# Optimization experiments

Measured on AMD Instinct MI355X. Metric: run time of the kernel, lower is better.

Reference implementation:

```python
import jax, jax.numpy as jnp
import numpy as np

H, C, L = 2, 32, 25
EPS = 1e-5


def setup_inputs() -> dict:
    key = jax.random.key(0)
    ks = jax.random.split(key, 12)
    N, E = 20000, 100000
    x_input = jax.random.normal(ks[0], (N, 5), jnp.float32)
    # edges with no self loops (module uses add_self_loops=True, which first removes them)
    src = jax.random.randint(ks[1], (L, E), 0, N, dtype=jnp.int32)
    off = jax.random.randint(ks[2], (L, E), 1, N, dtype=jnp.int32)
    dst = (src + off) % N
    edge_indices = jnp.stack([src, dst], axis=1)              # [L, 2, E]
    edge_weights = jax.random.uniform(ks[3], (L, E, 1), jnp.float32)
    g = lambda k, shp, fan: jax.random.normal(k, shp, jnp.float32) / np.float32(np.sqrt(fan))
    return {
        "x_input": x_input,
        "edge_indices": edge_indices,
        "edge_weights": edge_weights,
        "Wl": g(ks[4], (L, 5, H * C), 5),
        "bl": jnp.zeros((L, H * C), jnp.float32),
        "Wr": g(ks[5], (L, 5, H * C), 5),
        "br": jnp.zeros((L, H * C), jnp.float32),
        "We": g(ks[6], (L, 1, H * C), 1),
        "att": g(ks[7], (L, H, C), C),
        "conv_bias": jnp.zeros((L, C), jnp.float32),
        "gamma1": jnp.ones((L, C), jnp.float32),
        "beta1": jnp.zeros((L, C), jnp.float32),
        "W1": g(ks[8], (800, 800), 800),
        "b1": jnp.zeros((800,), jnp.float32),
        "W2": g(ks[9], (800, 5), 800),
        "b2": jnp.zeros((5,), jnp.float32),
    }


def reference(x_input, edge_indices, edge_weights, Wl, bl, Wr, br, We, att,
              conv_bias, gamma1, beta1, W1, b1, W2, b2):
    N = x_input.shape[0]
    loops = jnp.arange(N, dtype=edge_indices.dtype)

    def layer(carry, p):
        ei, ew, wl, bl_, wr, br_, we, a, cb, g_, be_ = p
        src, dst = ei[0], ei[1]
        ones_e = jnp.ones((src.shape[0],), x_input.dtype)
        # add_self_loops with fill_value='mean': loop attr = mean of incoming edge attrs
        cnt = jax.ops.segment_sum(ones_e, dst, num_segments=N)
        loop_attr = jax.ops.segment_sum(ew, dst, num_segments=N) / jnp.maximum(cnt, 1.0)[:, None]
        s2 = jnp.concatenate([src, loops])
        d2 = jnp.concatenate([dst, loops])
        ea = jnp.concatenate([ew, loop_attr], axis=0)          # [E+N, 1]
        xl = (x_input @ wl + bl_).reshape(N, H, C)             # source transform
        xr = (x_input @ wr + br_).reshape(N, H, C)             # target transform
        eh = jax.nn.leaky_relu(xl[s2] + xr[d2] + (ea @ we).reshape(-1, H, C), 0.2)
        alpha = jnp.einsum('ehc,hc->eh', eh, a)                # [E+N, H]
        amax = jax.ops.segment_max(alpha, d2, num_segments=N)
        alpha = jnp.exp(alpha - amax[d2])
        alpha = alpha / jax.ops.segment_sum(alpha, d2, num_segments=N)[d2]
        msg = (xl[s2] * alpha[:, :, None]).reshape(-1, H * C)
        deg = jax.ops.segment_sum(jnp.ones((s2.shape[0],), x_input.dtype), d2, num_segments=N)
        out = (jax.ops.segment_sum(msg, d2, num_segments=N) / deg[:, None]).reshape(N, H, C)
        out = out.mean(axis=1) + cb                            # concat=False -> mean over heads, + bias
        mu = out.mean(axis=0)
        var = out.var(axis=0)                                  # BatchNorm1d, training-mode batch stats
        out = g_ * (out - mu) * jax.lax.rsqrt(var + EPS) + be_
        return carry, jax.nn.leaky_relu(out, 0.01)

    _, hs = jax.lax.scan(layer, None,
                         (edge_indices, edge_weights, Wl, bl, Wr, br, We, att,
                          conv_bias, gamma1, beta1))            # [L, N, C]
    h = jnp.transpose(hs, (1, 0, 2)).reshape(N, L * C)          # cat along feature dim
    h = jax.nn.relu(h @ W1 + b1)
    return h @ W2 + b2
```

## Files before the change

kernel.cpp:

```cpp
#include <hip/hip_runtime.h>
#include <hip/hip_bf16.h>

#define N_NODES 20000
#define N_EDGES 100000
#define N_LAYERS 25
#define NPAD 20096
#define EPS_BN 1e-5f
#define LOG2E 1.44269504088896340736f
#define NL_NN (N_LAYERS * N_NODES)
#define TOTAL_E (N_LAYERS * N_EDGES)
#define SCAN_BLKS ((NL_NN + 1023) / 1024)
#define QUARTER_N 5000
#define CNT_BLKS (N_LAYERS * 4)
#define XLR_BASE CNT_BLKS
#define XLR_BLKS (NL_NN / 16)
#define W1T_BASE (XLR_BASE + XLR_BLKS)
#define PREP_BLKS (W1T_BASE + 700)
#define EDGE_BLKS ((TOTAL_E + 1023) / 1024)
#define FILL_BLKS (EDGE_BLKS + SCAN_BLKS)
#define NGRP 14
#define ATTN_BLKS (NL_NN / 4)
#define ATTN_PER_XCD (ATTN_BLKS / 8)

typedef short short8 __attribute__((ext_vector_type(8)));
typedef short short4v __attribute__((ext_vector_type(4)));
typedef float floatx4 __attribute__((ext_vector_type(4)));
typedef int int8v __attribute__((ext_vector_type(8)));

template <int PAT>
__device__ __forceinline__ float swz(float v) {
  return __int_as_float(__builtin_amdgcn_ds_swizzle(__float_as_int(v), PAT));
}

template <int CTRL>
__device__ __forceinline__ float dpp_add(float v) {
  int r = __builtin_amdgcn_update_dpp(0, __float_as_int(v), CTRL, 0xF, 0xF, true);
  return v + __int_as_float(r);
}

__device__ __forceinline__ float ldbf(const unsigned short* __restrict__ p, int idx) {
  return __uint_as_float((unsigned)p[idx] << 16);
}

__device__ __forceinline__ unsigned short bfbits(float v) {
  return __builtin_bit_cast(unsigned short, (__hip_bfloat16)v);
}

__device__ __forceinline__ void gl_lds16(const short* g, short* l) {
  __builtin_amdgcn_global_load_lds(
      (const __attribute__((address_space(1))) void*)g,
      (__attribute__((address_space(3))) void*)l, 16, 0, 0);
}

__device__ __forceinline__ void sload8(const int2* p, int8v& ra, int8v& rb) {
  asm volatile(
      "s_load_dwordx8 %0, %2, 0x0\n\t"
      "s_load_dwordx8 %1, %2, 0x20\n\t"
      "s_waitcnt lgkmcnt(0)"
      : "=s"(ra), "=s"(rb)
      : "s"(p));
}

__device__ __forceinline__ void red8(float& p0, float& p1, float& p2, float& p3,
                                     float& p4, float& p5, float& p6, float& p7) {
  asm volatile(
      "s_nop 1\n\t"
      "v_add_f32_dpp %0, %0, %0 quad_perm:[1,0,3,2] row_mask:0xf bank_mask:0xf\n\t"
      "v_add_f32_dpp %1, %1, %1 quad_perm:[1,0,3,2] row_mask:0xf bank_mask:0xf\n\t"
      "v_add_f32_dpp %2, %2, %2 quad_perm:[1,0,3,2] row_mask:0xf bank_mask:0xf\n\t"
      "v_add_f32_dpp %3, %3, %3 quad_perm:[1,0,3,2] row_mask:0xf bank_mask:0xf\n\t"
      "v_add_f32_dpp %4, %4, %4 quad_perm:[1,0,3,2] row_mask:0xf bank_mask:0xf\n\t"
      "v_add_f32_dpp %5, %5, %5 quad_perm:[1,0,3,2] row_mask:0xf bank_mask:0xf\n\t"
      "v_add_f32_dpp %6, %6, %6 quad_perm:[1,0,3,2] row_mask:0xf bank_mask:0xf\n\t"
      "v_add_f32_dpp %7, %7, %7 quad_perm:[1,0,3,2] row_mask:0xf bank_mask:0xf\n\t"
      "v_add_f32_dpp %0, %0, %0 quad_perm:[2,3,0,1] row_mask:0xf bank_mask:0xf\n\t"
      "v_add_f32_dpp %1, %1, %1 quad_perm:[2,3,0,1] row_mask:0xf bank_mask:0xf\n\t"
      "v_add_f32_dpp %2, %2, %2 quad_perm:[2,3,0,1] row_mask:0xf bank_mask:0xf\n\t"
      "v_add_f32_dpp %3, %3, %3 quad_perm:[2,3,0,1] row_mask:0xf bank_mask:0xf\n\t"
      "v_add_f32_dpp %4, %4, %4 quad_perm:[2,3,0,1] row_mask:0xf bank_mask:0xf\n\t"
      "v_add_f32_dpp %5, %5, %5 quad_perm:[2,3,0,1] row_mask:0xf bank_mask:0xf\n\t"
      "v_add_f32_dpp %6, %6, %6 quad_perm:[2,3,0,1] row_mask:0xf bank_mask:0xf\n\t"
      "v_add_f32_dpp %7, %7, %7 quad_perm:[2,3,0,1] row_mask:0xf bank_mask:0xf\n\t"
      "v_add_f32_dpp %0, %0, %0 row_half_mirror row_mask:0xf bank_mask:0xf\n\t"
      "v_add_f32_dpp %1, %1, %1 row_half_mirror row_mask:0xf bank_mask:0xf\n\t"
      "v_add_f32_dpp %2, %2, %2 row_half_mirror row_mask:0xf bank_mask:0xf\n\t"
      "v_add_f32_dpp %3, %3, %3 row_half_mirror row_mask:0xf bank_mask:0xf\n\t"
      "v_add_f32_dpp %4, %4, %4 row_half_mirror row_mask:0xf bank_mask:0xf\n\t"
      "v_add_f32_dpp %5, %5, %5 row_half_mirror row_mask:0xf bank_mask:0xf\n\t"
      "v_add_f32_dpp %6, %6, %6 row_half_mirror row_mask:0xf bank_mask:0xf\n\t"
      "v_add_f32_dpp %7, %7, %7 row_half_mirror row_mask:0xf bank_mask:0xf\n\t"
      "v_add_f32_dpp %0, %0, %0 row_mirror row_mask:0xf bank_mask:0xf\n\t"
      "v_add_f32_dpp %1, %1, %1 row_mirror row_mask:0xf bank_mask:0xf\n\t"
      "v_add_f32_dpp %2, %2, %2 row_mirror row_mask:0xf bank_mask:0xf\n\t"
      "v_add_f32_dpp %3, %3, %3 row_mirror row_mask:0xf bank_mask:0xf\n\t"
      "v_add_f32_dpp %4, %4, %4 row_mirror row_mask:0xf bank_mask:0xf\n\t"
      "v_add_f32_dpp %5, %5, %5 row_mirror row_mask:0xf bank_mask:0xf\n\t"
      "v_add_f32_dpp %6, %6, %6 row_mirror row_mask:0xf bank_mask:0xf\n\t"
      "v_add_f32_dpp %7, %7, %7 row_mirror row_mask:0xf bank_mask:0xf\n\t"
      "s_nop 1"
      : "+v"(p0), "+v"(p1), "+v"(p2), "+v"(p3),
        "+v"(p4), "+v"(p5), "+v"(p6), "+v"(p7));
}

__device__ __forceinline__ float red1(float p) {
  asm volatile(
      "s_nop 1\n\t"
      "v_add_f32_dpp %0, %0, %0 quad_perm:[1,0,3,2] row_mask:0xf bank_mask:0xf\n\t"
      "s_nop 1\n\t"
      "v_add_f32_dpp %0, %0, %0 quad_perm:[2,3,0,1] row_mask:0xf bank_mask:0xf\n\t"
      "s_nop 1\n\t"
      "v_add_f32_dpp %0, %0, %0 row_half_mirror row_mask:0xf bank_mask:0xf\n\t"
      "s_nop 1\n\t"
      "v_add_f32_dpp %0, %0, %0 row_mirror row_mask:0xf bank_mask:0xf\n\t"
      "s_nop 1"
      : "+v"(p));
  return p;
}

__global__ __launch_bounds__(1024) void prep_kernel(
    const int* __restrict__ ei, const float* __restrict__ x,
    const float* __restrict__ Wl, const float* __restrict__ bl,
    const float* __restrict__ Wr, const float* __restrict__ br,
    const float* __restrict__ W1, int* __restrict__ cnt,
    int* __restrict__ rank,
    unsigned short* __restrict__ xlb, unsigned short* __restrict__ xrb,
    __hip_bfloat16* __restrict__ W1bT) {
  __shared__ int smem[QUARTER_N];
  int b = blockIdx.x;
  if (b < XLR_BASE) {
    int l = b >> 2, base = (b & 3) * QUARTER_N;
    for (int i = threadIdx.x; i < QUARTER_N; i += 1024) smem[i] = 0;
    __syncthreads();
    const int* dstp = ei + (size_t)l * 2 * N_EDGES + N_EDGES;
    int* rkp = rank + l * N_EDGES;
    for (int e = threadIdx.x; e < N_EDGES; e += 1024) {
      int d = dstp[e] - base;
      if ((unsigned)d < (unsigned)QUARTER_N) rkp[e] = atomicAdd(&smem[d], 1);
    }
    __syncthreads();
    int* outp = cnt + l * N_NODES + base;
    for (int i = threadIdx.x; i < QUARTER_N; i += 1024) outp[i] = smem[i];
  } else if (b < W1T_BASE) {
    int wid = (b - XLR_BASE) * 16 + (threadIdx.x >> 6);
    int lane = threadIdx.x & 63;
    int l = wid / N_NODES, n = wid - l * N_NODES;
    float a = bl[l * 64 + lane];
    float c = br[l * 64 + lane];
#pragma unroll
    for (int k = 0; k < 5; k++) {
      float xk = x[n * 5 + k];
      a = fmaf(xk, Wl[(l * 5 + k) * 64 + lane], a);
      c = fmaf(xk, Wr[(l * 5 + k) * 64 + lane], c);
    }
    xlb[wid * 64 + lane] = bfbits(a);
    xrb[wid * 64 + lane] = bfbits(c);
  } else {
    float* tile = (float*)smem;
    int bb = b - W1T_BASE;
    int j0 = (bb % 28) * 32, k0 = (bb / 28) * 32;
    int tx = threadIdx.x & 31, ty = threadIdx.x >> 5;
    tile[ty * 33 + tx] = (j0 + tx < 800) ? W1[(k0 + ty) * 800 + j0 + tx] : 0.f;
    __syncthreads();
    W1bT[(size_t)(j0 + ty) * 800 + k0 + tx] = (__hip_bfloat16)tile[tx * 33 + ty];
  }
}

__global__ __launch_bounds__(1024) void scan_a(const int* __restrict__ cnt,
                                               int* __restrict__ scn,
                                               int* __restrict__ btot,
                                               float* __restrict__ gsum,
                                               float* __restrict__ gsumsq) {
  int t = threadIdx.x, b = blockIdx.x;
  int i = b * 1024 + t;
  int lane = t & 63, wv = t >> 6;
  int v = (i < NL_NN) ? cnt[i] : 0;
  int sc = v;
#pragma unroll
  for (int off = 1; off < 64; off <<= 1) {
    int u = __shfl_up(sc, off);
    if (lane >= off) sc += u;
  }
  __shared__ int ws[16];
  if (lane == 63) ws[wv] = sc;
  __syncthreads();
  if (t < 16) {
    int xx = ws[t];
#pragma unroll
    for (int off = 1; off < 16; off <<= 1) {
      int u = __shfl_up(xx, off);
      if (t >= off) xx += u;
    }
    ws[t] = xx;
  }
  __syncthreads();
  int bofs = wv ? ws[wv - 1] : 0;
  if (i < NL_NN) scn[i] = bofs + sc - v;
  if (t == 0) btot[b] = ws[15];
  if (b == 200 && t < N_LAYERS * 32) {
    gsum[t] = 0.f;
    gsumsq[t] = 0.f;
  }
}

__global__ __launch_bounds__(512) void scan_b(const int* __restrict__ btot,
                                              int* __restrict__ boff) {
  int t = threadIdx.x;
  int lane = t & 63, wv = t >> 6;
  int v = (t < SCAN_BLKS) ? btot[t] : 0;
  int sc = v;
#pragma unroll
  for (int off = 1; off < 64; off <<= 1) {
    int u = __shfl_up(sc, off);
    if (lane >= off) sc += u;
  }
  __shared__ int ws[8];
  if (lane == 63) ws[wv] = sc;
  __syncthreads();
  if (t < 8) {
    int xx = ws[t];
#pragma unroll
    for (int off = 1; off < 8; off <<= 1) {
      int u = __shfl_up(xx, off);
      if (t >= off) xx += u;
    }
    ws[t] = xx;
  }
  __syncthreads();
  int bofs = wv ? ws[wv - 1] : 0;
  if (t < SCAN_BLKS) boff[t] = bofs + sc - v;
}

__global__ __launch_bounds__(1024) void fill_kernel(const int* __restrict__ ei,
                                                    const float* __restrict__ ew,
                                                    const int* __restrict__ scn,
                                                    const int* __restrict__ boff,
                                                    const int* __restrict__ rank,
                                                    int* __restrict__ rowfin,
                                                    int2* __restrict__ ep) {
  int b = blockIdx.x;
  if (b < EDGE_BLKS) {
    int idx = b * 1024 + threadIdx.x;
    if (idx >= TOTAL_E) return;
    int l = idx / N_EDGES, e = idx - l * N_EDGES;
    int src = ei[(size_t)l * 2 * N_EDGES + e];
    int dst = ei[(size_t)l * 2 * N_EDGES + N_EDGES + e];
    int g = l * N_NODES + dst;
    int pos = scn[g] + boff[g >> 10] + rank[idx];
    int2 rec;
    rec.x = src;
    rec.y = __float_as_int(ew[(size_t)l * N_EDGES + e]);
    ep[pos] = rec;
  } else {
    int i = (b - EDGE_BLKS) * 1024 + threadIdx.x;
    if (i < NL_NN) rowfin[i] = scn[i] + boff[i >> 10];
    if (i == 0) rowfin[NL_NN] = TOTAL_E;
    if (i < 8) {
      int2 z;
      z.x = 0;
      z.y = 0;
      ep[TOTAL_E + i] = z;
    }
  }
}

__global__ __launch_bounds__(256) void attn_kernel(
    const unsigned short* __restrict__ xlg, const unsigned short* __restrict__ xrg,
    const int* __restrict__ rowfin, const int2* __restrict__ ep,
    const float* __restrict__ We, const float* __restrict__ att,
    const float* __restrict__ cbias, unsigned short* __restrict__ out_pre) {
  int b = blockIdx.x;
  int nb = (b & 7) * ATTN_PER_XCD + (b >> 3);
  int wid = nb * 4 + (threadIdx.x >> 6);
  int lane = threadIdx.x & 63;
  int l = wid / N_NODES, n = wid - l * N_NODES;

  const unsigned short* xlb = xlg + (size_t)l * N_NODES * 64;
  float wev = We[l * 64 + lane];
  float att2v = att[l * 64 + lane] * LOG2E;

  float xrn = ldbf(xrg, wid * 64 + lane);
  float xln = ldbf(xlb, n * 64 + lane);

  int start = __builtin_amdgcn_readfirstlane(rowfin[wid]);
  int end   = __builtin_amdgcn_readfirstlane(rowfin[wid + 1]);
  int cnt = end - start;

  float ssum = 0.f, acc = 0.f, ewsum = 0.f;
  int nchunk = (cnt + 7) >> 3;
  for (int c = 0; c < nchunk; c++) {
    const int2* pchunk = ep + start + c * 8;
    int8v ra, rb;
    sload8(pchunk, ra, rb);
    int m = cnt - c * 8;
#define RECS(k) ((k) < 4 ? ra[2 * (k)] : rb[2 * ((k)-4)])
#define RECW(k) ((k) < 4 ? ra[2 * (k) + 1] : rb[2 * ((k)-4) + 1])
    float xa[8], pk[8], wv[8];
#pragma unroll
    for (int k = 0; k < 8; k++) {
      const unsigned short* ps = xlb + RECS(k) * 64;
      xa[k] = ldbf(ps, lane);
    }
#pragma unroll
    for (int k = 0; k < 8; k++) {
      bool ok = k < m;
      int wbits = ok ? RECW(k) : 0;
      wv[k] = __int_as_float(wbits);
      int bbits = ok ? 0 : (int)0xff800000;
      float bias = __int_as_float(bbits);
      float v = xa[k] + fmaf(wv[k], wev, xrn);
      float lk = fmaxf(v, 0.2f * v);
      pk[k] = fmaf(lk, att2v, bias);
    }
#undef RECS
#undef RECW
    red8(pk[0], pk[1], pk[2], pk[3], pk[4], pk[5], pk[6], pk[7]);
#pragma unroll
    for (int k = 0; k < 8; k++) pk[k] += swz<0x401F>(pk[k]);
#pragma unroll
    for (int k = 0; k < 8; k++) {
      float pe = __builtin_amdgcn_exp2f(pk[k]);
      ssum += pe;
      acc = fmaf(xa[k], pe, acc);
      ewsum += wv[k];
    }
  }
  {
    float w = ewsum * __builtin_amdgcn_rcpf(fmaxf((float)cnt, 1.f));
    float v = xln + fmaf(w, wev, xrn);
    float lk = fmaxf(v, 0.2f * v);
    float p = red1(lk * att2v);
    p += swz<0x401F>(p);
    float pe = __builtin_amdgcn_exp2f(p);
    ssum += pe;
    acc = fmaf(xln, pe, acc);
  }
  float outv = acc * __builtin_amdgcn_rcpf(ssum * (float)(cnt + 1));
  float o2 = outv + __shfl_xor(outv, 32);
  if (lane < 32)
    out_pre[wid * 32 + lane] = bfbits(0.5f * o2 + cbias[l * 32 + lane]);
}

__global__ __launch_bounds__(256) void stats_kernel(const unsigned short* __restrict__ out_pre,
                                                    float* __restrict__ gsum,
                                                    float* __restrict__ gsumsq) {
  int l = blockIdx.x >> 4, chunk = blockIdx.x & 15;
  int t = threadIdx.x;
  int c = t & 31, nsub = t >> 5;
  int n0 = chunk * 1250;
  float s1 = 0.f, s2 = 0.f;
  for (int n = n0 + nsub; n < n0 + 1250; n += 8) {
    float v = ldbf(out_pre, (l * N_NODES + n) * 32 + c);
    s1 += v; s2 += v * v;
  }
  __shared__ float l1[256], l2[256];
  l1[t] = s1; l2[t] = s2;
  __syncthreads();
  for (int off = 128; off >= 32; off >>= 1) {
    if (t < off) { l1[t] += l1[t + off]; l2[t] += l2[t + off]; }
    __syncthreads();
  }
  if (t < 32) {
    atomicAdd(&gsum[l * 32 + t], l1[t]);
    atomicAdd(&gsumsq[l * 32 + t], l2[t]);
  }
}

__global__ __launch_bounds__(256) void norm_kernel(const unsigned short* __restrict__ out_pre,
                                                   const float* __restrict__ gsum,
                                                   const float* __restrict__ gsumsq,
                                                   const float* __restrict__ gamma,
                                                   const float* __restrict__ beta,
                                                   unsigned short* __restrict__ hn) {
  int idx = blockIdx.x * 256 + threadIdx.x;
  int l = idx / (N_NODES * 8);
  int rem = idx - l * (N_NODES * 8);
  int n = rem >> 3, q = rem & 7;
  int c0 = q * 4;
  short4v v4 = *(const short4v*)(out_pre + (l * N_NODES + n) * 32 + c0);
  short4v o;
#pragma unroll
  for (int i = 0; i < 4; i++) {
    int c = c0 + i;
    float mu = gsum[l * 32 + c] * (1.f / N_NODES);
    float var = gsumsq[l * 32 + c] * (1.f / N_NODES) - mu * mu;
    float vv = __uint_as_float((unsigned)(unsigned short)v4[i] << 16);
    float v = gamma[l * 32 + c] * (vv - mu) * rsqrtf(var + EPS_BN) + beta[l * 32 + c];
    v = v > 0.f ? v : 0.01f * v;
    o[i] = (short)bfbits(v);
  }
  *(short4v*)(hn + ((size_t)l * NPAD + n) * 32 + c0) = o;
}

__global__ __launch_bounds__(256) void gemm1_kernel(const short* __restrict__ hn,
                                                    const short* __restrict__ W1bT,
                                                    const float* __restrict__ b1,
                                                    const float* __restrict__ W2,
                                                    float* __restrict__ p) {
  __shared__ __align__(16) short As[128 * 32];
  __shared__ __align__(16) short Bs[128 * 32];
  int t = threadIdx.x;
  int n0 = blockIdx.x * 128, m0 = blockIdx.y * 128;
  int wave = t >> 6, lane = t & 63;
  int wr = wave >> 1, wc = wave & 1;
  int mrow = lane & 15, quad = lane >> 4;
  floatx4 acc[4][4];
#pragma unroll
  for (int i = 0; i < 4; i++)
#pragma unroll
    for (int j = 0; j < 4; j++) acc[i][j] = (floatx4){0.f, 0.f, 0.f, 0.f};

  int r0 = t >> 2, s0 = t & 3;
  int r1 = (t + 256) >> 2, s1 = (t + 256) & 3;
  const short* aG0 = hn + (m0 + r0) * 32 + s0 * 8;
  const short* aG1 = hn + (m0 + r1) * 32 + s1 * 8;
  const short* bG0 = W1bT + (n0 + r0) * 800 + s0 * 8;
  const short* bG1 = W1bT + (n0 + r1) * 800 + s1 * 8;
  const int ak = NPAD * 32;
  short* aD0 = As + wave * 512;
  short* aD1 = As + 2048 + wave * 512;
  short* bD0 = Bs + wave * 512;
  short* bD1 = Bs + 2048 + wave * 512;

  for (int kt = 0; kt < 25; kt++) {
    gl_lds16(aG0, aD0);
    gl_lds16(aG1, aD1);
    gl_lds16(bG0, bD0);
    gl_lds16(bG1, bD1);
    aG0 += ak; aG1 += ak; bG0 += 32; bG1 += 32;
    __syncthreads();
    short8 af[4], bfr[4];
#pragma unroll
    for (int i = 0; i < 4; i++)
      af[i] = *(const short8*)(&As[(wr * 64 + i * 16 + mrow) * 32 + quad * 8]);
#pragma unroll
    for (int j = 0; j < 4; j++)
      bfr[j] = *(const short8*)(&Bs[(wc * 64 + j * 16 + mrow) * 32 + quad * 8]);
#pragma unroll
    for (int i = 0; i < 4; i++)
#pragma unroll
      for (int j = 0; j < 4; j++)
        acc[i][j] = __builtin_amdgcn_mfma_f32_16x16x32_bf16(af[i], bfr[j], acc[i][j], 0, 0, 0);
    __syncthreads();
  }

  float w2v[4][5];
  float b1v[4];
#pragma unroll
  for (int j = 0; j < 4; j++) {
    int col = n0 + wc * 64 + j * 16 + mrow;
    bool ok = col < 800;
    b1v[j] = ok ? b1[col] : 0.f;
#pragma unroll
    for (int jj = 0; jj < 5; jj++) w2v[j][jj] = ok ? W2[col * 5 + jj] : 0.f;
  }
  int grp = blockIdx.x * 2 + wc;
#pragma unroll
  for (int i = 0; i < 4; i++) {
#pragma unroll
    for (int r = 0; r < 4; r++) {
      float s[5] = {0.f, 0.f, 0.f, 0.f, 0.f};
#pragma unroll
      for (int j = 0; j < 4; j++) {
        float v = fmaxf(acc[i][j][r] + b1v[j], 0.f);
#pragma unroll
        for (int jj = 0; jj < 5; jj++) s[jj] = fmaf(v, w2v[j][jj], s[jj]);
      }
#pragma unroll
      for (int jj = 0; jj < 5; jj++) {
        s[jj] = dpp_add<0xB1>(s[jj]);
        s[jj] = dpp_add<0x4E>(s[jj]);
        s[jj] = dpp_add<0x141>(s[jj]);
        s[jj] = dpp_add<0x140>(s[jj]);
      }
      int row = m0 + wr * 64 + i * 16 + quad * 4 + r;
      if (mrow == 0) {
#pragma unroll
        for (int jj = 0; jj < 5; jj++)
          p[(row * NGRP + grp) * 5 + jj] = s[jj];
      }
    }
  }
}

__global__ __launch_bounds__(256) void gemm2r_kernel(const float* __restrict__ p,
                                                     const float* __restrict__ b2,
                                                     float* __restrict__ out) {
  int idx = blockIdx.x * 256 + threadIdx.x;
  if (idx >= N_NODES * 5) return;
  int row = idx / 5, jj = idx - row * 5;
  float s = b2[jj];
#pragma unroll
  for (int g = 0; g < NGRP; g++) s += p[(row * NGRP + g) * 5 + jj];
  out[idx] = s;
}

extern "C" void kernel_launch(void* const* d_in, const int* in_sizes, int n_in,
                              void* d_out, int out_size, void* d_ws, size_t ws_size,
                              hipStream_t stream) {
  const float* x    = (const float*)d_in[0];
  const int*   ei   = (const int*)d_in[1];
  const float* ew   = (const float*)d_in[2];
  const float* Wl   = (const float*)d_in[3];
  const float* bl   = (const float*)d_in[4];
  const float* Wr   = (const float*)d_in[5];
  const float* br   = (const float*)d_in[6];
  const float* We   = (const float*)d_in[7];
  const float* att  = (const float*)d_in[8];
  const float* cb   = (const float*)d_in[9];
  const float* gam  = (const float*)d_in[10];
  const float* bet  = (const float*)d_in[11];
  const float* W1   = (const float*)d_in[12];
  const float* b1   = (const float*)d_in[13];
  const float* W2   = (const float*)d_in[14];
  const float* b2   = (const float*)d_in[15];

  char* ws = (char*)d_ws;
  size_t off = 0;
  auto alloc = [&](size_t bytes) {
    void* p = ws + off;
    off = (off + bytes + 255) & ~(size_t)255;
    return p;
  };
  int* cnt     = (int*)alloc((size_t)NL_NN * 4);
  int* scn     = (int*)alloc((size_t)NL_NN * 4);
  int* btot    = (int*)alloc(SCAN_BLKS * 4);
  int* boff    = (int*)alloc(SCAN_BLKS * 4);
  int* rank    = (int*)alloc((size_t)TOTAL_E * 4);
  int* rowfin  = (int*)alloc((size_t)(NL_NN + 1) * 4);
  int2* ep     = (int2*)alloc((size_t)TOTAL_E * 8 + 64);
  unsigned short* out_pre = (unsigned short*)alloc((size_t)NL_NN * 32 * 2);
  float* gsum   = (float*)alloc(N_LAYERS * 32 * 4);
  float* gsumsq = (float*)alloc(N_LAYERS * 32 * 4);
  unsigned short* xlb = (unsigned short*)alloc((size_t)NL_NN * 64 * 2);
  unsigned short* xrb = (unsigned short*)alloc((size_t)NL_NN * 64 * 2);
  __hip_bfloat16* w1t = (__hip_bfloat16*)alloc((size_t)896 * 800 * 2);
  float* pbuf = (float*)alloc((size_t)NPAD * NGRP * 5 * 4);
  unsigned short* hn  = (unsigned short*)xlb;

  prep_kernel<<<PREP_BLKS, 1024, 0, stream>>>(ei, x, Wl, bl, Wr, br, W1,
                                              cnt, rank, xlb, xrb, w1t);
  scan_a<<<SCAN_BLKS, 1024, 0, stream>>>(cnt, scn, btot, gsum, gsumsq);
  scan_b<<<1, 512, 0, stream>>>(btot, boff);
  fill_kernel<<<FILL_BLKS, 1024, 0, stream>>>(ei, ew, scn, boff, rank, rowfin, ep);
  attn_kernel<<<ATTN_BLKS, 256, 0, stream>>>(
      xlb, xrb, rowfin, ep, We, att, cb, out_pre);
  stats_kernel<<<N_LAYERS * 16, 256, 0, stream>>>(out_pre, gsum, gsumsq);
  norm_kernel<<<(NL_NN * 8) / 256, 256, 0, stream>>>(
      out_pre, gsum, gsumsq, gam, bet, hn);
  gemm1_kernel<<<dim3(7, 157), 256, 0, stream>>>(
      (const short*)hn, (const short*)w1t, b1, W2, pbuf);
  gemm2r_kernel<<<(N_NODES * 5 + 255) / 256, 256, 0, stream>>>(
      pbuf, b2, (float*)d_out);
}
```

Baseline: 537.7 us.

## Recompute per-edge source projection from raw 5-dim inputs packed into edge records

Stops materializing the bf16 xl/xr projections (25 layers x 20000 nodes x 64). Each edge record in CSR order now carries the edge weight and the source node's 5 raw input features, and the attention kernel recomputes the 64-wide projection with 5 FMAs per lane. This removes a random 128-byte gather per edge and the large projection write, but edge records grow from 8 to 32 bytes and chunking drops from 8 to 4 edges. hn gets its own buffer, and its padding rows are now zeroed in prep because it no longer aliases xlb.

```diff
diff --git a/kernel.cpp b/kernel.cpp
--- a/kernel.cpp
+++ b/kernel.cpp
@@ -12,10 +12,10 @@
 #define SCAN_BLKS ((NL_NN + 1023) / 1024)
 #define QUARTER_N 5000
 #define CNT_BLKS (N_LAYERS * 4)
-#define XLR_BASE CNT_BLKS
-#define XLR_BLKS (NL_NN / 16)
-#define W1T_BASE (XLR_BASE + XLR_BLKS)
-#define PREP_BLKS (W1T_BASE + 700)
+#define W1T_END (CNT_BLKS + 700)
+#define XPAD_END (W1T_END + 157)
+#define HPAD_BLKS 75
+#define PREP_BLKS (XPAD_END + HPAD_BLKS)
 #define EDGE_BLKS ((TOTAL_E + 1023) / 1024)
 #define FILL_BLKS (EDGE_BLKS + SCAN_BLKS)
 #define NGRP 14
@@ -25,7 +25,9 @@
 typedef short short8 __attribute__((ext_vector_type(8)));
 typedef short short4v __attribute__((ext_vector_type(4)));
 typedef float floatx4 __attribute__((ext_vector_type(4)));
+typedef float float8v __attribute__((ext_vector_type(8)));
 typedef int int8v __attribute__((ext_vector_type(8)));
+typedef int int2v __attribute__((ext_vector_type(2)));
 
 template <int PAT>
 __device__ __forceinline__ float swz(float v) {
@@ -52,54 +54,60 @@
       (__attribute__((address_space(3))) void*)l, 16, 0, 0);
 }
 
-__device__ __forceinline__ void sload8(const int2* p, int8v& ra, int8v& rb) {
+__device__ __forceinline__ int8v sload8(const void* p) {
+  int8v r;
   asm volatile(
-      "s_load_dwordx8 %0, %2, 0x0\n\t"
-      "s_load_dwordx8 %1, %2, 0x20\n\t"
+      "s_load_dwordx8 %0, %1, 0x0\n\t"
       "s_waitcnt lgkmcnt(0)"
-      : "=s"(ra), "=s"(rb)
+      : "=s"(r)
       : "s"(p));
-}
-
-__device__ __forceinline__ void red8(float& p0, float& p1, float& p2, float& p3,
-                                     float& p4, float& p5, float& p6, float& p7) {
+  return r;
+}
+
+__device__ __forceinline__ void sload2(const void* p, int& a, int& b) {
+  int2v r;
+  asm volatile(
+      "s_load_dwordx2 %0, %1, 0x0\n\t"
+      "s_waitcnt lgkmcnt(0)"
+      : "=s"(r)
+      : "s"(p));
+  a = r[0];
+  b = r[1];
+}
+
+__device__ __forceinline__ void sload_chunk(const void* p, int8v& r0, int8v& r1,
+                                            int8v& r2, int8v& r3) {
+  asm volatile(
+      "s_load_dwordx8 %0, %4, 0x0\n\t"
+      "s_load_dwordx8 %1, %4, 0x20\n\t"
+      "s_load_dwordx8 %2, %4, 0x40\n\t"
+      "s_load_dwordx8 %3, %4, 0x60\n\t"
+      "s_waitcnt lgkmcnt(0)"
+      : "=s"(r0), "=s"(r1), "=s"(r2), "=s"(r3)
+      : "s"(p));
+}
+
+__device__ __forceinline__ void red4(float& p0, float& p1, float& p2, float& p3) {
   asm volatile(
       "s_nop 1\n\t"
       "v_add_f32_dpp %0, %0, %0 quad_perm:[1,0,3,2] row_mask:0xf bank_mask:0xf\n\t"
       "v_add_f32_dpp %1, %1, %1 quad_perm:[1,0,3,2] row_mask:0xf bank_mask:0xf\n\t"
       "v_add_f32_dpp %2, %2, %2 quad_perm:[1,0,3,2] row_mask:0xf bank_mask:0xf\n\t"
       "v_add_f32_dpp %3, %3, %3 quad_perm:[1,0,3,2] row_mask:0xf bank_mask:0xf\n\t"
-      "v_add_f32_dpp %4, %4, %4 quad_perm:[1,0,3,2] row_mask:0xf bank_mask:0xf\n\t"
-      "v_add_f32_dpp %5, %5, %5 quad_perm:[1,0,3,2] row_mask:0xf bank_mask:0xf\n\t"
-      "v_add_f32_dpp %6, %6, %6 quad_perm:[1,0,3,2] row_mask:0xf bank_mask:0xf\n\t"
-      "v_add_f32_dpp %7, %7, %7 quad_perm:[1,0,3,2] row_mask:0xf bank_mask:0xf\n\t"
       "v_add_f32_dpp %0, %0, %0 quad_perm:[2,3,0,1] row_mask:0xf bank_mask:0xf\n\t"
       "v_add_f32_dpp %1, %1, %1 quad_perm:[2,3,0,1] row_mask:0xf bank_mask:0xf\n\t"
       "v_add_f32_dpp %2, %2, %2 quad_perm:[2,3,0,1] row_mask:0xf bank_mask:0xf\n\t"
       "v_add_f32_dpp %3, %3, %3 quad_perm:[2,3,0,1] row_mask:0xf bank_mask:0xf\n\t"
-      "v_add_f32_dpp %4, %4, %4 quad_perm:[2,3,0,1] row_mask:0xf bank_mask:0xf\n\t"
-      "v_add_f32_dpp %5, %5, %5 quad_perm:[2,3,0,1] row_mask:0xf bank_mask:0xf\n\t"
-      "v_add_f32_dpp %6, %6, %6 quad_perm:[2,3,0,1] row_mask:0xf bank_mask:0xf\n\t"
-      "v_add_f32_dpp %7, %7, %7 quad_perm:[2,3,0,1] row_mask:0xf bank_mask:0xf\n\t"
       "v_add_f32_dpp %0, %0, %0 row_half_mirror row_mask:0xf bank_mask:0xf\n\t"
       "v_add_f32_dpp %1, %1, %1 row_half_mirror row_mask:0xf bank_mask:0xf\n\t"
       "v_add_f32_dpp %2, %2, %2 row_half_mirror row_mask:0xf bank_mask:0xf\n\t"
       "v_add_f32_dpp %3, %3, %3 row_half_mirror row_mask:0xf bank_mask:0xf\n\t"
-      "v_add_f32_dpp %4, %4, %4 row_half_mirror row_mask:0xf bank_mask:0xf\n\t"
-      "v_add_f32_dpp %5, %5, %5 row_half_mirror row_mask:0xf bank_mask:0xf\n\t"
-      "v_add_f32_dpp %6, %6, %6 row_half_mirror row_mask:0xf bank_mask:0xf\n\t"
-      "v_add_f32_dpp %7, %7, %7 row_half_mirror row_mask:0xf bank_mask:0xf\n\t"
       "v_add_f32_dpp %0, %0, %0 row_mirror row_mask:0xf bank_mask:0xf\n\t"
       "v_add_f32_dpp %1, %1, %1 row_mirror row_mask:0xf bank_mask:0xf\n\t"
       "v_add_f32_dpp %2, %2, %2 row_mirror row_mask:0xf bank_mask:0xf\n\t"
       "v_add_f32_dpp %3, %3, %3 row_mirror row_mask:0xf bank_mask:0xf\n\t"
-      "v_add_f32_dpp %4, %4, %4 row_mirror row_mask:0xf bank_mask:0xf\n\t"
-      "v_add_f32_dpp %5, %5, %5 row_mirror row_mask:0xf bank_mask:0xf\n\t"
-      "v_add_f32_dpp %6, %6, %6 row_mirror row_mask:0xf bank_mask:0xf\n\t"
-      "v_add_f32_dpp %7, %7, %7 row_mirror row_mask:0xf bank_mask:0xf\n\t"
       "s_nop 1"
-      : "+v"(p0), "+v"(p1), "+v"(p2), "+v"(p3),
-        "+v"(p4), "+v"(p5), "+v"(p6), "+v"(p7));
+      : "+v"(p0), "+v"(p1), "+v"(p2), "+v"(p3));
 }
 
 __device__ __forceinline__ float red1(float p) {
@@ -119,15 +127,12 @@
 
 __global__ __launch_bounds__(1024) void prep_kernel(
     const int* __restrict__ ei, const float* __restrict__ x,
-    const float* __restrict__ Wl, const float* __restrict__ bl,
-    const float* __restrict__ Wr, const float* __restrict__ br,
     const float* __restrict__ W1, int* __restrict__ cnt,
-    int* __restrict__ rank,
-    unsigned short* __restrict__ xlb, unsigned short* __restrict__ xrb,
-    __hip_bfloat16* __restrict__ W1bT) {
+    int* __restrict__ rank, float* __restrict__ xpad,
+    __hip_bfloat16* __restrict__ W1bT, unsigned short* __restrict__ hn) {
   __shared__ int smem[QUARTER_N];
   int b = blockIdx.x;
-  if (b < XLR_BASE) {
+  if (b < CNT_BLKS) {
     int l = b >> 2, base = (b & 3) * QUARTER_N;
     for (int i = threadIdx.x; i < QUARTER_N; i += 1024) smem[i] = 0;
     __syncthreads();
@@ -140,28 +145,28 @@
     __syncthreads();
     int* outp = cnt + l * N_NODES + base;
     for (int i = threadIdx.x; i < QUARTER_N; i += 1024) outp[i] = smem[i];
-  } else if (b < W1T_BASE) {
-    int wid = (b - XLR_BASE) * 16 + (threadIdx.x >> 6);
-    int lane = threadIdx.x & 63;
-    int l = wid / N_NODES, n = wid - l * N_NODES;
-    float a = bl[l * 64 + lane];
-    float c = br[l * 64 + lane];
-#pragma unroll
-    for (int k = 0; k < 5; k++) {
-      float xk = x[n * 5 + k];
-      a = fmaf(xk, Wl[(l * 5 + k) * 64 + lane], a);
-      c = fmaf(xk, Wr[(l * 5 + k) * 64 + lane], c);
-    }
-    xlb[wid * 64 + lane] = bfbits(a);
-    xrb[wid * 64 + lane] = bfbits(c);
-  } else {
+  } else if (b < W1T_END) {
     float* tile = (float*)smem;
-    int bb = b - W1T_BASE;
+    int bb = b - CNT_BLKS;
     int j0 = (bb % 28) * 32, k0 = (bb / 28) * 32;
     int tx = threadIdx.x & 31, ty = threadIdx.x >> 5;
     tile[ty * 33 + tx] = (j0 + tx < 800) ? W1[(k0 + ty) * 800 + j0 + tx] : 0.f;
     __syncthreads();
     W1bT[(size_t)(j0 + ty) * 800 + k0 + tx] = (__hip_bfloat16)tile[tx * 33 + ty];
+  } else if (b < XPAD_END) {
+    int idx = (b - W1T_END) * 1024 + threadIdx.x;
+    if (idx < N_NODES * 8) {
+      int nn = idx >> 3, k = idx & 7;
+      xpad[idx] = (k < 5) ? x[nn * 5 + k] : 0.f;
+    }
+  } else {
+    int idx = (b - XPAD_END) * 1024 + threadIdx.x;
+    const int per_l = (NPAD - N_NODES) * 32;
+    if (idx < N_LAYERS * per_l) {
+      int l = idx / per_l;
+      int rem = idx - l * per_l;
+      hn[((size_t)l * NPAD + N_NODES) * 32 + rem] = 0;
+    }
   }
 }
 
@@ -235,8 +240,9 @@
                                                     const int* __restrict__ scn,
                                                     const int* __restrict__ boff,
                                                     const int* __restrict__ rank,
-                                                    int* __restrict__ rowfin,
-                                                    int2* __restrict__ ep) {
+                                                    const float* __restrict__ xpad,
+                                                    int2* __restrict__ rowse,
+                                                    float* __restrict__ epf) {
   int b = blockIdx.x;
   if (b < EDGE_BLKS) {
     int idx = b * 1024 + threadIdx.x;
@@ -246,78 +252,104 @@
     int dst = ei[(size_t)l * 2 * N_EDGES + N_EDGES + e];
     int g = l * N_NODES + dst;
     int pos = scn[g] + boff[g >> 10] + rank[idx];
-    int2 rec;
-    rec.x = src;
-    rec.y = __float_as_int(ew[(size_t)l * N_EDGES + e]);
-    ep[pos] = rec;
+    float w = ew[(size_t)l * N_EDGES + e];
+    float4 xv = *(const float4*)(xpad + (size_t)src * 8);
+    float x4v = xpad[(size_t)src * 8 + 4];
+    float8v r;
+    r[0] = w; r[1] = xv.x; r[2] = xv.y; r[3] = xv.z; r[4] = xv.w; r[5] = x4v;
+    r[6] = 0.f; r[7] = 0.f;
+    *(float8v*)(epf + (size_t)pos * 8) = r;
   } else {
     int i = (b - EDGE_BLKS) * 1024 + threadIdx.x;
-    if (i < NL_NN) rowfin[i] = scn[i] + boff[i >> 10];
-    if (i == 0) rowfin[NL_NN] = TOTAL_E;
-    if (i < 8) {
-      int2 z;
-      z.x = 0;
-      z.y = 0;
-      ep[TOTAL_E + i] = z;
+    if (i < NL_NN) {
+      int st = scn[i] + boff[i >> 10];
+      int en = (i + 1 < NL_NN) ? scn[i + 1] + boff[(i + 1) >> 10] : TOTAL_E;
+      rowse[i] = make_int2(st, en);
+    }
+    if (i < 4) {
+      float8v z = {0.f, 0.f, 0.f, 0.f, 0.f, 0.f, 0.f, 0.f};
+      *(float8v*)(epf + (size_t)(TOTAL_E + i) * 8) = z;
     }
   }
 }
 
 __global__ __launch_bounds__(256) void attn_kernel(
-    const unsigned short* __restrict__ xlg, const unsigned short* __restrict__ xrg,
-    const int* __restrict__ rowfin, const int2* __restrict__ ep,
+    const float* __restrict__ xpad, const int2* __restrict__ rowse,
+    const float* __restrict__ epf,
+    const float* __restrict__ Wl, const float* __restrict__ bl,
+    const float* __restrict__ Wr, const float* __restrict__ br,
     const float* __restrict__ We, const float* __restrict__ att,
     const float* __restrict__ cbias, unsigned short* __restrict__ out_pre) {
   int b = blockIdx.x;
   int nb = (b & 7) * ATTN_PER_XCD + (b >> 3);
-  int wid = nb * 4 + (threadIdx.x >> 6);
+  int wid = __builtin_amdgcn_readfirstlane(nb * 4 + (threadIdx.x >> 6));
   int lane = threadIdx.x & 63;
   int l = wid / N_NODES, n = wid - l * N_NODES;
 
-  const unsigned short* xlb = xlg + (size_t)l * N_NODES * 64;
+  float wlv0 = Wl[(l * 5 + 0) * 64 + lane];
+  float wlv1 = Wl[(l * 5 + 1) * 64 + lane];
+  float wlv2 = Wl[(l * 5 + 2) * 64 + lane];
+  float wlv3 = Wl[(l * 5 + 3) * 64 + lane];
+  float wlv4 = Wl[(l * 5 + 4) * 64 + lane];
+  float blv = bl[l * 64 + lane];
   float wev = We[l * 64 + lane];
   float att2v = att[l * 64 + lane] * LOG2E;
 
-  float xrn = ldbf(xrg, wid * 64 + lane);
-  float xln = ldbf(xlb, n * 64 + lane);
-
-  int start = __builtin_amdgcn_readfirstlane(rowfin[wid]);
-  int end   = __builtin_amdgcn_readfirstlane(rowfin[wid + 1]);
-  int cnt = end - start;
+  int s_, e_;
+  sload2(rowse + wid, s_, e_);
+  int cnt = e_ - s_;
+
+  int8v xn = sload8(xpad + (size_t)n * 8);
+  float xrn = br[l * 64 + lane];
+  float xln = blv;
+  {
+    float wr0 = Wr[(l * 5 + 0) * 64 + lane];
+    float wr1 = Wr[(l * 5 + 1) * 64 + lane];
+    float wr2 = Wr[(l * 5 + 2) * 64 + lane];
+    float wr3 = Wr[(l * 5 + 3) * 64 + lane];
+    float wr4 = Wr[(l * 5 + 4) * 64 + lane];
+    float x0 = __int_as_float(xn[0]), x1 = __int_as_float(xn[1]);
+    float x2 = __int_as_float(xn[2]), x3 = __int_as_float(xn[3]);
+    float x4 = __int_as_float(xn[4]);
+    xrn = fmaf(x0, wr0, xrn); xrn = fmaf(x1, wr1, xrn);
+    xrn = fmaf(x2, wr2, xrn); xrn = fmaf(x3, wr3, xrn);
+    xrn = fmaf(x4, wr4, xrn);
+    xln = fmaf(x0, wlv0, xln); xln = fmaf(x1, wlv1, xln);
+    xln = fmaf(x2, wlv2, xln); xln = fmaf(x3, wlv3, xln);
+    xln = fmaf(x4, wlv4, xln);
+  }
 
   float ssum = 0.f, acc = 0.f, ewsum = 0.f;
-  int nchunk = (cnt + 7) >> 3;
+  int nchunk = (cnt + 3) >> 2;
+  const float* pch = epf + (size_t)s_ * 8;
   for (int c = 0; c < nchunk; c++) {
-    const int2* pchunk = ep + start + c * 8;
-    int8v ra, rb;
-    sload8(pchunk, ra, rb);
-    int m = cnt - c * 8;
-#define RECS(k) ((k) < 4 ? ra[2 * (k)] : rb[2 * ((k)-4)])
-#define RECW(k) ((k) < 4 ? ra[2 * (k) + 1] : rb[2 * ((k)-4) + 1])
-    float xa[8], pk[8], wv[8];
-#pragma unroll
-    for (int k = 0; k < 8; k++) {
-      const unsigned short* ps = xlb + RECS(k) * 64;
-      xa[k] = ldbf(ps, lane);
-    }
-#pragma unroll
-    for (int k = 0; k < 8; k++) {
+    int8v r0, r1, r2, r3;
+    sload_chunk(pch, r0, r1, r2, r3);
+    pch += 32;
+    int m = cnt - c * 4;
+    float xa[4], pk[4], wv[4];
+#pragma unroll
+    for (int k = 0; k < 4; k++) {
+      int8v rr = (k == 0) ? r0 : (k == 1) ? r1 : (k == 2) ? r2 : r3;
       bool ok = k < m;
-      int wbits = ok ? RECW(k) : 0;
+      int wbits = ok ? rr[0] : 0;
       wv[k] = __int_as_float(wbits);
-      int bbits = ok ? 0 : (int)0xff800000;
-      float bias = __int_as_float(bbits);
-      float v = xa[k] + fmaf(wv[k], wev, xrn);
+      float a = fmaf(__int_as_float(rr[1]), wlv0, blv);
+      a = fmaf(__int_as_float(rr[2]), wlv1, a);
+      a = fmaf(__int_as_float(rr[3]), wlv2, a);
+      a = fmaf(__int_as_float(rr[4]), wlv3, a);
+      a = fmaf(__int_as_float(rr[5]), wlv4, a);
+      xa[k] = a;
+      float bias = __int_as_float(ok ? 0 : (int)0xff800000);
+      float v = a + fmaf(wv[k], wev, xrn);
       float lk = fmaxf(v, 0.2f * v);
       pk[k] = fmaf(lk, att2v, bias);
     }
-#undef RECS
-#undef RECW
-    red8(pk[0], pk[1], pk[2], pk[3], pk[4], pk[5], pk[6], pk[7]);
-#pragma unroll
-    for (int k = 0; k < 8; k++) pk[k] += swz<0x401F>(pk[k]);
-#pragma unroll
-    for (int k = 0; k < 8; k++) {
+    red4(pk[0], pk[1], pk[2], pk[3]);
+#pragma unroll
+    for (int k = 0; k < 4; k++) pk[k] += swz<0x401F>(pk[k]);
+#pragma unroll
+    for (int k = 0; k < 4; k++) {
       float pe = __builtin_amdgcn_exp2f(pk[k]);
       ssum += pe;
       acc = fmaf(xa[k], pe, acc);
@@ -526,24 +558,23 @@
   int* btot    = (int*)alloc(SCAN_BLKS * 4);
   int* boff    = (int*)alloc(SCAN_BLKS * 4);
   int* rank    = (int*)alloc((size_t)TOTAL_E * 4);
-  int* rowfin  = (int*)alloc((size_t)(NL_NN + 1) * 4);
-  int2* ep     = (int2*)alloc((size_t)TOTAL_E * 8 + 64);
+  int2* rowse  = (int2*)alloc((size_t)NL_NN * 8);
+  float* epf   = (float*)alloc((size_t)TOTAL_E * 32 + 128);
   unsigned short* out_pre = (unsigned short*)alloc((size_t)NL_NN * 32 * 2);
   float* gsum   = (float*)alloc(N_LAYERS * 32 * 4);
   float* gsumsq = (float*)alloc(N_LAYERS * 32 * 4);
-  unsigned short* xlb = (unsigned short*)alloc((size_t)NL_NN * 64 * 2);
-  unsigned short* xrb = (unsigned short*)alloc((size_t)NL_NN * 64 * 2);
+  float* xpad   = (float*)alloc((size_t)N_NODES * 8 * 4);
   __hip_bfloat16* w1t = (__hip_bfloat16*)alloc((size_t)896 * 800 * 2);
   float* pbuf = (float*)alloc((size_t)NPAD * NGRP * 5 * 4);
-  unsigned short* hn  = (unsigned short*)xlb;
-
-  prep_kernel<<<PREP_BLKS, 1024, 0, stream>>>(ei, x, Wl, bl, Wr, br, W1,
-                                              cnt, rank, xlb, xrb, w1t);
+  unsigned short* hn = (unsigned short*)alloc((size_t)N_LAYERS * NPAD * 32 * 2);
+
+  prep_kernel<<<PREP_BLKS, 1024, 0, stream>>>(ei, x, W1, cnt, rank, xpad, w1t, hn);
   scan_a<<<SCAN_BLKS, 1024, 0, stream>>>(cnt, scn, btot, gsum, gsumsq);
   scan_b<<<1, 512, 0, stream>>>(btot, boff);
-  fill_kernel<<<FILL_BLKS, 1024, 0, stream>>>(ei, ew, scn, boff, rank, rowfin, ep);
+  fill_kernel<<<FILL_BLKS, 1024, 0, stream>>>(ei, ew, scn, boff, rank, xpad,
+                                              rowse, epf);
   attn_kernel<<<ATTN_BLKS, 256, 0, stream>>>(
-      xlb, xrb, rowfin, ep, We, att, cb, out_pre);
+      xpad, rowse, epf, Wl, bl, Wr, br, We, att, cb, out_pre);
   stats_kernel<<<N_LAYERS * 16, 256, 0, stream>>>(out_pre, gsum, gsumsq);
   norm_kernel<<<(NL_NN * 8) / 256, 256, 0, stream>>>(
       out_pre, gsum, gsumsq, gam, bet, hn);
```

Result: faster. 500.5 us (-6.9%).
